# Optimization experiments

Hardware: AMD Instinct MI355X
Metric: run time of the kernel (lower is better)

Reference implementation:

```python
import jax, jax.numpy as jnp
import numpy as np

D_MODEL = 1024
N_HEADS = 16
D_HEAD = D_MODEL // N_HEADS
WIN = 256
NEG_INF = -1e30


def setup_inputs() -> dict:
    key = jax.random.key(0)
    k1, k2, k3 = jax.random.split(key, 3)
    B, L = 4, 4096
    x = jax.random.normal(k1, (B, L, D_MODEL), dtype=jnp.float32)
    w_qkv = jax.random.normal(k2, (D_MODEL, 3 * D_MODEL), dtype=jnp.float32) * (1.0 / np.sqrt(D_MODEL))
    w_out = jax.random.normal(k3, (D_MODEL, D_MODEL), dtype=jnp.float32) * (1.0 / np.sqrt(D_MODEL))
    return {"x": x, "w_qkv": w_qkv, "w_out": w_out}


def _band_mask(nb: int):
    ti = jnp.arange(WIN)[:, None]
    tj = jnp.arange(2 * WIN)[None, :]
    base = (tj >= ti + 1) & (tj <= ti + WIN)
    first = base & (tj >= WIN)                         # block 0 has zero-padded (invalid) prev block
    rest = jnp.broadcast_to(base, (nb - 1, WIN, 2 * WIN))
    return jnp.concatenate([first[None], rest], axis=0)


def reference(x, w_qkv, w_out):
    B, L, D = x.shape
    nb = L // WIN
    qkv = (x @ w_qkv).reshape(B, L, 3, N_HEADS, D_HEAD)
    q, k, v = qkv[:, :, 0], qkv[:, :, 1], qkv[:, :, 2]          # [B, L, H, dh]
    def to_blocks(t):
        return t.transpose(0, 2, 1, 3).reshape(B, N_HEADS, nb, WIN, D_HEAD)
    qb, kb, vb = to_blocks(q), to_blocks(k), to_blocks(v)
    zero_blk = jnp.zeros_like(kb[:, :, :1])
    k_kv = jnp.concatenate([jnp.concatenate([zero_blk, kb[:, :, :-1]], axis=2), kb], axis=3)  # [B,H,nb,2W,dh]
    v_kv = jnp.concatenate([jnp.concatenate([zero_blk, vb[:, :, :-1]], axis=2), vb], axis=3)
    scale = 1.0 / np.sqrt(D_HEAD)
    scores = jnp.einsum('bhnqd,bhnkd->bhnqk', qb, k_kv) * scale
    scores = jnp.where(_band_mask(nb), scores, NEG_INF)
    attn = jax.nn.softmax(scores, axis=-1)
    ob = jnp.einsum('bhnqk,bhnkd->bhnqd', attn, v_kv)
    out = ob.reshape(B, N_HEADS, L, D_HEAD).transpose(0, 2, 1, 3).reshape(B, L, D)
    return out @ w_out
```

## Files before the change

kernel.cpp:

```cpp
#include <hip/hip_runtime.h>

typedef __bf16 bf16_t;
typedef __bf16 bf16x8 __attribute__((ext_vector_type(8)));
typedef float f32x4 __attribute__((ext_vector_type(4)));
typedef unsigned short ushort_t;

#define MFMA_16x16x32(a, b, c) __builtin_amdgcn_mfma_f32_16x16x32_bf16((a), (b), (c), 0, 0, 0)

__device__ __forceinline__ void async_ld16(const void* gptr, void* lptr) {
  typedef __attribute__((address_space(1))) const unsigned int as1_t;
  typedef __attribute__((address_space(3))) unsigned int as3_t;
  __builtin_amdgcn_global_load_lds((as1_t*)(unsigned long long)gptr,
                                   (as3_t*)(unsigned int)(unsigned long long)lptr,
                                   16, 0, 0);
}

__global__ void detect_dtype(const ushort_t* __restrict__ x, int* __restrict__ flag) {
  __shared__ int cnt[256];
  int c = 0;
#pragma unroll
  for (int i = 0; i < 16; ++i) {
    const ushort_t u = x[threadIdx.x * 16 + i];
    const int e = (u >> 7) & 0xFF;
    if ((u & 0x7FFF) != 0 && (e < 0x3A || e > 0xC0)) ++c;
  }
  cnt[threadIdx.x] = c;
  __syncthreads();
  if (threadIdx.x == 0) {
    int t = 0;
    for (int i = 0; i < 256; ++i) t += cnt[i];
    *flag = (t > 512) ? 1 : 0;
  }
}

__global__ __launch_bounds__(256) void convert_to_bf16(const void* __restrict__ src,
                                                       bf16_t* __restrict__ dst, int n8,
                                                       const int* __restrict__ flag) {
  const int isF32 = *flag;
  int i = blockIdx.x * 256 + threadIdx.x;
  const int stride = gridDim.x * 256;
  if (isF32) {
    const float4* s = (const float4*)src;
    for (; i < n8; i += stride) {
      const float4 a = s[(size_t)i * 2];
      const float4 b = s[(size_t)i * 2 + 1];
      bf16x8 o;
      o[0] = (bf16_t)a.x; o[1] = (bf16_t)a.y; o[2] = (bf16_t)a.z; o[3] = (bf16_t)a.w;
      o[4] = (bf16_t)b.x; o[5] = (bf16_t)b.y; o[6] = (bf16_t)b.z; o[7] = (bf16_t)b.w;
      *(bf16x8*)(dst + (size_t)i * 8) = o;
    }
  } else {
    const uint4* s = (const uint4*)src;
    for (; i < n8; i += stride) ((uint4*)dst)[i] = s[i];
  }
}

__global__ __launch_bounds__(256) void transpose_b16(const ushort_t* __restrict__ in,
                                                     ushort_t* __restrict__ out,
                                                     int R, int C) {
  __shared__ alignas(16) ushort_t t[64 * 72];
  const int tid = threadIdx.x;
  const int c0 = blockIdx.x * 64;
  const int r0 = blockIdx.y * 64;
#pragma unroll
  for (int it = 0; it < 2; ++it) {
    int cid = tid + it * 256;
    int row = cid >> 3, co = (cid & 7) * 8;
    *(uint4*)(t + row * 72 + co) = *(const uint4*)(in + (size_t)(r0 + row) * C + c0 + co);
  }
  __syncthreads();
#pragma unroll
  for (int it = 0; it < 2; ++it) {
    int cid = tid + it * 256;
    int orow = cid >> 3, ko = (cid & 7) * 8;
    uint4 u;
    ushort_t* tp = (ushort_t*)&u;
#pragma unroll
    for (int j = 0; j < 8; ++j) tp[j] = t[(ko + j) * 72 + orow];
    *(uint4*)(out + (size_t)(c0 + orow) * R + r0 + ko) = u;
  }
}

__global__ __launch_bounds__(256) void transpose_v(const ushort_t* __restrict__ qkv,
                                                   ushort_t* __restrict__ vT) {
  __shared__ alignas(16) ushort_t t[64 * 72];
  const int tid = threadIdx.x;
  const int l0 = blockIdx.x * 64;
  const int bh = blockIdx.y;
  const int b = bh >> 4, h = bh & 15;
  const ushort_t* src = qkv + ((size_t)(b * 4096 + l0)) * 3072 + 2048 + h * 64;
#pragma unroll
  for (int it = 0; it < 2; ++it) {
    int cid = tid + it * 256;
    int row = cid >> 3, co = (cid & 7) * 8;
    *(uint4*)(t + row * 72 + co) = *(const uint4*)(src + (size_t)row * 3072 + co);
  }
  __syncthreads();
  ushort_t* dst = vT + ((size_t)bh * 64) * 4096 + l0;
#pragma unroll
  for (int it = 0; it < 2; ++it) {
    int cid = tid + it * 256;
    int d = cid >> 3, ko = (cid & 7) * 8;
    uint4 u;
    ushort_t* tp = (ushort_t*)&u;
#pragma unroll
    for (int j = 0; j < 8; ++j) tp[j] = t[(ko + j) * 72 + d];
    *(uint4*)(dst + (size_t)d * 4096 + ko) = u;
  }
}

__global__ __launch_bounds__(512) void gemm_bf16(const bf16_t* __restrict__ A, int lda,
                                                 const bf16_t* __restrict__ Bt,
                                                 void* __restrict__ Cout, int N_out,
                                                 int K, const int* __restrict__ flag) {
  __shared__ alignas(16) bf16_t smem[49152];
  const int tid = threadIdx.x;
  const int wave = tid >> 6;
  const int lane = tid & 63;
  const int l15 = lane & 15;
  const int quad = lane >> 4;
  const int wm = wave >> 2;
  const int wn = wave & 3;

  int lin = blockIdx.y * gridDim.x + blockIdx.x;
  const int nwg = gridDim.x * gridDim.y;
  if ((nwg & 7) == 0) lin = (lin & 7) * (nwg >> 3) + (lin >> 3);
  const int tn = (lin % gridDim.x) * 256;
  const int tm = (lin / gridDim.x) * 256;

  f32x4 acc[8][4];
#pragma unroll
  for (int i = 0; i < 8; ++i)
#pragma unroll
    for (int j = 0; j < 4; ++j) acc[i][j] = (f32x4){0.f, 0.f, 0.f, 0.f};

  const int r_st = tid >> 2;
  const int csrc = ((tid & 3) ^ ((tid >> 3) & 3)) * 8;
  const int wofs = wave * 512;

  const int rowA = wm * 16 + l15;
  const int rowB = wn * 16 + l15;
  const int cfr = (quad ^ ((l15 >> 1) & 3)) * 8;

  const int NT = K >> 5;

#define STAGE_HALF(G, ldg, grow0, kk, base)                                  \
  async_ld16((G) + (size_t)((grow0) + r_st) * (ldg) + (kk) + csrc,           \
             &smem[(base) + wofs])

#define STAGE4(kk, base)                                \
  do {                                                  \
    STAGE_HALF(A, lda, tm, (kk), (base));               \
    STAGE_HALF(Bt, K, tn, (kk), (base) + 8192);         \
    STAGE_HALF(Bt, K, tn + 128, (kk), (base) + 12288);  \
    STAGE_HALF(A, lda, tm + 128, (kk), (base) + 4096);  \
  } while (0)

  STAGE4(0, 0);
  STAGE4(32, 16384);
  asm volatile("s_waitcnt vmcnt(4)" ::: "memory");
  __builtin_amdgcn_s_barrier();

  int rb = 0;
  for (int t = 0; t < NT; ++t) {
    const int kst = (t + 2) << 5;
    const bool pf = (kst < K);
    const int sb = (rb >= 16384) ? rb - 16384 : rb + 32768;
    if (pf) STAGE4(kst, sb);

    bf16x8 a_[8], b_[4];
#pragma unroll
    for (int mh = 0; mh < 2; ++mh)
#pragma unroll
      for (int q = 0; q < 4; ++q)
        a_[mh * 4 + q] = *(const bf16x8*)&smem[rb + mh * 4096 +
                                               ((q * 32 + rowA) << 5) + cfr];
#pragma unroll
    for (int nh = 0; nh < 2; ++nh)
#pragma unroll
      for (int jn = 0; jn < 2; ++jn)
        b_[nh * 2 + jn] = *(const bf16x8*)&smem[rb + 8192 + nh * 4096 +
                                                ((jn * 64 + rowB) << 5) + cfr];

    __builtin_amdgcn_s_setprio(1);
#pragma unroll
    for (int f = 0; f < 8; ++f)
#pragma unroll
      for (int n = 0; n < 4; ++n) acc[f][n] = MFMA_16x16x32(a_[f], b_[n], acc[f][n]);
    __builtin_amdgcn_s_setprio(0);

    asm volatile("s_waitcnt vmcnt(4)" ::: "memory");
    if (!pf) asm volatile("s_waitcnt vmcnt(0)" ::: "memory");
    __builtin_amdgcn_s_barrier();
    rb = (rb == 32768) ? 0 : rb + 16384;
  }

  __syncthreads();

  const int isF32 = flag ? *flag : 0;
  if (isF32) {
#pragma unroll
    for (int f = 0; f < 8; ++f) {
      const int m0 = tm + (f >> 2) * 128 + (f & 3) * 32 + wm * 16 + quad * 4;
#pragma unroll
      for (int nidx = 0; nidx < 4; ++nidx) {
        const int col = tn + (nidx >> 1) * 128 + (nidx & 1) * 64 + wn * 16 + l15;
        float* cp = (float*)Cout + (size_t)m0 * N_out + col;
#pragma unroll
        for (int r = 0; r < 4; ++r) cp[(size_t)r * N_out] = acc[f][nidx][r];
      }
    }
  } else {
    bf16_t* stg = smem + wave * 1152;
#pragma unroll
    for (int f = 0; f < 8; ++f) {
#pragma unroll
      for (int nidx = 0; nidx < 4; ++nidx)
#pragma unroll
        for (int r = 0; r < 4; ++r)
          stg[(quad * 4 + r) * 72 + nidx * 16 + l15] = (bf16_t)acc[f][nidx][r];
      __asm__ volatile("s_waitcnt lgkmcnt(0)" ::: "memory");
      const int m0 = tm + (f >> 2) * 128 + (f & 3) * 32 + wm * 16;
#pragma unroll
      for (int p = 0; p < 2; ++p) {
        const int idx = lane + p * 64;
        const int row = idx >> 3, c8 = (idx & 7) * 8;
        uint4 u = *(const uint4*)(stg + row * 72 + c8);
        const int col = tn + ((c8 >> 5) << 7) + (((c8 >> 4) & 1) << 6) + wn * 16 + (c8 & 15);
        *(uint4*)((bf16_t*)Cout + (size_t)(m0 + row) * N_out + col) = u;
      }
      __asm__ volatile("s_waitcnt lgkmcnt(0)" ::: "memory");
    }
  }
#undef STAGE_HALF
#undef STAGE4
}

__global__ __launch_bounds__(256) void attn_swa(bf16_t* qkv, const bf16_t* __restrict__ vT) {
  __shared__ alignas(16) bf16_t k_lds[64 * 72];
  __shared__ alignas(16) bf16_t vt_lds[64 * 72];
  __shared__ alignas(16) bf16_t p_lds[4 * 16 * 72];

  int wg = blockIdx.x;
  wg = (wg & 7) * 512 + (wg >> 3);
  const int b = wg >> 10;
  const int h = (wg >> 6) & 15;
  const int qt = wg & 63;
  const int blk = qt >> 2;
  const int wq = qt & 3;
  const int tid = threadIdx.x;
  const int wave = tid >> 6;
  const int lane = tid & 63;
  const int l15 = lane & 15;
  const int quad = lane >> 4;
  const int qw = qt * 64 + wave * 16;

  const size_t qoff = ((size_t)(b * 4096 + qw + l15)) * 3072 + h * 64;
  const bf16x8 qf0 = *(const bf16x8*)(qkv + qoff + quad * 8);
  const bf16x8 qf1 = *(const bf16x8*)(qkv + qoff + 32 + quad * 8);

  f32x4 of[4];
#pragma unroll
  for (int i = 0; i < 4; ++i) of[i] = (f32x4){0.f, 0.f, 0.f, 0.f};
  float m_i[4], l_i[4];
#pragma unroll
  for (int r = 0; r < 4; ++r) {
    m_i[r] = -1e30f;
    l_i[r] = 0.0f;
  }

  const int kb0 = blk * 256 - 256;
  const int kclo = (blk == 0) ? 4 : wq;
  const int kchi = wq + 4;

  const int row0 = tid >> 3;
  const int co8 = (tid & 7) * 8;
  const bf16_t* kbase = qkv + ((size_t)b * 4096) * 3072 + 1024 + h * 64;
  const bf16_t* vbase = vT + (((size_t)b * 16 + h) * 64) * 4096;
  uint4 kr0, kr1, vr0, vr1;

#define ISSUE_KV(KB)                                                           \
  do {                                                                         \
    kr0 = *(const uint4*)(kbase + (size_t)((KB) + row0) * 3072 + co8);         \
    kr1 = *(const uint4*)(kbase + (size_t)((KB) + row0 + 32) * 3072 + co8);    \
    vr0 = *(const uint4*)(vbase + (size_t)row0 * 4096 + (KB) + co8);           \
    vr1 = *(const uint4*)(vbase + (size_t)(row0 + 32) * 4096 + (KB) + co8);    \
  } while (0)

  ISSUE_KV(kb0 + kclo * 64);

  for (int kc = kclo; kc <= kchi; ++kc) {
    const int kb = kb0 + kc * 64;
    __syncthreads();
    *(uint4*)(k_lds + row0 * 72 + co8) = kr0;
    *(uint4*)(k_lds + (row0 + 32) * 72 + co8) = kr1;
    *(uint4*)(vt_lds + row0 * 72 + co8) = vr0;
    *(uint4*)(vt_lds + (row0 + 32) * 72 + co8) = vr1;
    if (kc < kchi) ISSUE_KV(kb + 64);
    __syncthreads();

    f32x4 s[4];
    __builtin_amdgcn_s_setprio(1);
#pragma unroll
    for (int nt = 0; nt < 4; ++nt) {
      bf16x8 kf0 = *(const bf16x8*)(k_lds + (nt * 16 + l15) * 72 + quad * 8);
      bf16x8 kf1 = *(const bf16x8*)(k_lds + (nt * 16 + l15) * 72 + 32 + quad * 8);
      f32x4 z = (f32x4){0.f, 0.f, 0.f, 0.f};
      z = MFMA_16x16x32(qf0, kf0, z);
      z = MFMA_16x16x32(qf1, kf1, z);
      s[nt] = z;
    }
    __builtin_amdgcn_s_setprio(0);

    const bool full = (kb + 63 <= qw) && (kb >= qw - 240);
    float sv[4][4];
    if (full) {
#pragma unroll
      for (int nt = 0; nt < 4; ++nt)
#pragma unroll
        for (int r = 0; r < 4; ++r) sv[nt][r] = s[nt][r] * 0.125f;
    } else {
#pragma unroll
      for (int nt = 0; nt < 4; ++nt) {
        const int key = kb + nt * 16 + l15;
#pragma unroll
        for (int r = 0; r < 4; ++r) {
          const int p = qw + quad * 4 + r;
          const bool valid = (key <= p) && (key + 256 > p);
          sv[nt][r] = valid ? s[nt][r] * 0.125f : -1e30f;
        }
      }
    }
    float rm[4];
#pragma unroll
    for (int r = 0; r < 4; ++r)
      rm[r] = fmaxf(fmaxf(sv[0][r], sv[1][r]), fmaxf(sv[2][r], sv[3][r]));
#pragma unroll
    for (int off = 1; off < 16; off <<= 1)
#pragma unroll
      for (int r = 0; r < 4; ++r) rm[r] = fmaxf(rm[r], __shfl_xor(rm[r], off));

    const bool dok = (rm[0] <= m_i[0] + 8.0f) && (rm[1] <= m_i[1] + 8.0f) &&
                     (rm[2] <= m_i[2] + 8.0f) && (rm[3] <= m_i[3] + 8.0f);
    const bool defer = __all((int)dok);
    float mn[4];
    if (defer) {
#pragma unroll
      for (int r = 0; r < 4; ++r) mn[r] = m_i[r];
    } else {
#pragma unroll
      for (int r = 0; r < 4; ++r) mn[r] = fmaxf(m_i[r], rm[r]);
    }

    float rs[4] = {0.f, 0.f, 0.f, 0.f};
#pragma unroll
    for (int nt = 0; nt < 4; ++nt)
#pragma unroll
      for (int r = 0; r < 4; ++r) {
        const float pv = __expf(sv[nt][r] - mn[r]);
        rs[r] += pv;
        p_lds[wave * 1152 + (quad * 4 + r) * 72 + nt * 16 + l15] = (bf16_t)pv;
      }
#pragma unroll
    for (int off = 1; off < 16; off <<= 1)
#pragma unroll
      for (int r = 0; r < 4; ++r) rs[r] += __shfl_xor(rs[r], off);

    if (defer) {
#pragma unroll
      for (int r = 0; r < 4; ++r) l_i[r] += rs[r];
    } else {
#pragma unroll
      for (int r = 0; r < 4; ++r) {
        const float alpha = __expf(m_i[r] - mn[r]);
        l_i[r] = l_i[r] * alpha + rs[r];
        m_i[r] = mn[r];
#pragma unroll
        for (int dt = 0; dt < 4; ++dt) of[dt][r] *= alpha;
      }
    }

    __builtin_amdgcn_s_setprio(1);
#pragma unroll
    for (int kk = 0; kk < 2; ++kk) {
      bf16x8 pf = *(const bf16x8*)(p_lds + wave * 1152 + l15 * 72 + kk * 32 + quad * 8);
#pragma unroll
      for (int dt = 0; dt < 4; ++dt) {
        bf16x8 vf = *(const bf16x8*)(vt_lds + (dt * 16 + l15) * 72 + kk * 32 + quad * 8);
        of[dt] = MFMA_16x16x32(pf, vf, of[dt]);
      }
    }
    __builtin_amdgcn_s_setprio(0);
  }
#undef ISSUE_KV

  float inv[4];
#pragma unroll
  for (int r = 0; r < 4; ++r) inv[r] = 1.0f / fmaxf(l_i[r], 1e-20f);
  bf16_t* op = qkv + ((size_t)(b * 4096 + qw)) * 3072 + h * 64;
#pragma unroll
  for (int dt = 0; dt < 4; ++dt)
#pragma unroll
    for (int r = 0; r < 4; ++r)
      op[(size_t)(quad * 4 + r) * 3072 + dt * 16 + l15] = (bf16_t)(of[dt][r] * inv[r]);
}

extern "C" void kernel_launch(void* const* d_in, const int* in_sizes, int n_in,
                              void* d_out, int out_size, void* d_ws, size_t ws_size,
                              hipStream_t stream) {
  char* ws = (char*)d_ws;
  bf16_t* wTq = (bf16_t*)(ws);
  bf16_t* wTo = (bf16_t*)(ws + 6291456);
  bf16_t* qkv = (bf16_t*)(ws + 8388608);
  int* flag = (int*)(ws + 109051904);

  bf16_t* xb = (bf16_t*)d_out;
  bf16_t* vTb = (bf16_t*)d_out;
  bf16_t* tmpq = qkv;
  bf16_t* tmpo = qkv + 3145728;

  detect_dtype<<<1, 256, 0, stream>>>((const ushort_t*)d_in[0], flag);
  convert_to_bf16<<<1024, 256, 0, stream>>>(d_in[0], xb, 2097152, flag);
  convert_to_bf16<<<512, 256, 0, stream>>>(d_in[1], tmpq, 393216, flag);
  convert_to_bf16<<<256, 256, 0, stream>>>(d_in[2], tmpo, 131072, flag);
  transpose_b16<<<dim3(48, 16), 256, 0, stream>>>((const ushort_t*)tmpq, (ushort_t*)wTq,
                                                  1024, 3072);
  transpose_b16<<<dim3(16, 16), 256, 0, stream>>>((const ushort_t*)tmpo, (ushort_t*)wTo,
                                                  1024, 1024);
  gemm_bf16<<<dim3(12, 64), 512, 0, stream>>>(xb, 1024, wTq, qkv, 3072, 1024, nullptr);
  transpose_v<<<dim3(64, 64), 256, 0, stream>>>((const ushort_t*)qkv, (ushort_t*)vTb);
  attn_swa<<<dim3(4096), 256, 0, stream>>>(qkv, vTb);
  gemm_bf16<<<dim3(4, 64), 512, 0, stream>>>(qkv, 3072, wTo, d_out, 1024, 1024, flag);
}
```

Measured before the change: 386.7 us.

## Use 128x128 tile GEMM for output projection and simplify attention softmax

Adds a new 128x128-tile, 256-thread bf16 GEMM kernel and uses it for the output projection, giving 1024 workgroups in place of 256 larger tiles, which raises occupancy and parallelism. The new kernel has a simple single-buffered K loop with two barriers per step and no pipelining. In the attention kernel it removes the full-tile fast path and the deferred max-rescale trick, so the online softmax now always rescales. Masked scores are explicitly zeroed. This adds extra exp and multiply work per iteration.

Measured after the change: 411.3 us. 6.4% more time.

```diff
diff --git a/kernel.cpp b/kernel.cpp
--- a/kernel.cpp
+++ b/kernel.cpp
@@ -236,6 +236,96 @@
 #undef STAGE4
 }
 
+__global__ __launch_bounds__(256) void gemm128_bf16(const bf16_t* __restrict__ A, int lda,
+                                                    const bf16_t* __restrict__ Bt,
+                                                    void* __restrict__ Cout, int N_out,
+                                                    int K, const int* __restrict__ flag) {
+  __shared__ alignas(16) bf16_t smem[8192];
+  bf16_t* a_lds = smem;
+  bf16_t* b_lds = smem + 4096;
+  const int tid = threadIdx.x;
+  const int wave = tid >> 6;
+  const int lane = tid & 63;
+  const int l15 = lane & 15;
+  const int quad = lane >> 4;
+  const int tm = blockIdx.y * 128;
+  const int tn = blockIdx.x * 128;
+  const int wm = (wave >> 1) * 64;
+  const int wn = (wave & 1) * 64;
+
+  f32x4 acc[4][4];
+#pragma unroll
+  for (int i = 0; i < 4; ++i)
+#pragma unroll
+    for (int j = 0; j < 4; ++j) acc[i][j] = (f32x4){0.f, 0.f, 0.f, 0.f};
+
+  const int srow = wave * 32 + (lane >> 2);
+  const int scol = (lane & 3) * 8;
+  const bf16_t* ag = A + (size_t)(tm + srow) * lda + scol;
+  const bf16_t* bg = Bt + (size_t)(tn + srow) * K + scol;
+  bf16_t* al = a_lds + (wave * 32) * 32;
+  bf16_t* bl = b_lds + (wave * 32) * 32;
+
+  for (int k0 = 0; k0 < K; k0 += 32) {
+    __syncthreads();
+    async_ld16(ag, al);
+    async_ld16(ag + (size_t)16 * lda, al + 16 * 32);
+    async_ld16(bg, bl);
+    async_ld16(bg + (size_t)16 * K, bl + 16 * 32);
+    ag += 32;
+    bg += 32;
+    __syncthreads();
+
+    bf16x8 af[4], bfr[4];
+#pragma unroll
+    for (int i = 0; i < 4; ++i)
+      af[i] = *(const bf16x8*)(a_lds + (wm + i * 16 + l15) * 32 + quad * 8);
+#pragma unroll
+    for (int j = 0; j < 4; ++j)
+      bfr[j] = *(const bf16x8*)(b_lds + (wn + j * 16 + l15) * 32 + quad * 8);
+#pragma unroll
+    for (int i = 0; i < 4; ++i)
+#pragma unroll
+      for (int j = 0; j < 4; ++j) acc[i][j] = MFMA_16x16x32(af[i], bfr[j], acc[i][j]);
+  }
+  __syncthreads();
+
+  const int isF32 = flag ? *flag : 0;
+  if (isF32) {
+#pragma unroll
+    for (int i = 0; i < 4; ++i) {
+      const int m = tm + wm + i * 16 + quad * 4;
+#pragma unroll
+      for (int j = 0; j < 4; ++j) {
+        const int n = tn + wn + j * 16 + l15;
+        float* cp = (float*)Cout + (size_t)m * N_out + n;
+#pragma unroll
+        for (int r = 0; r < 4; ++r) cp[(size_t)r * N_out] = acc[i][j][r];
+      }
+    }
+  } else {
+    bf16_t* stg = smem + wave * 1152;
+#pragma unroll
+    for (int i = 0; i < 4; ++i) {
+#pragma unroll
+      for (int j = 0; j < 4; ++j)
+#pragma unroll
+        for (int r = 0; r < 4; ++r)
+          stg[(quad * 4 + r) * 72 + j * 16 + l15] = (bf16_t)acc[i][j][r];
+      __asm__ volatile("s_waitcnt lgkmcnt(0)" ::: "memory");
+      const int m0 = tm + wm + i * 16;
+#pragma unroll
+      for (int p = 0; p < 2; ++p) {
+        const int idx = lane + p * 64;
+        const int row = idx >> 3, c8 = (idx & 7) * 8;
+        uint4 u = *(const uint4*)(stg + row * 72 + c8);
+        *(uint4*)((bf16_t*)Cout + (size_t)(m0 + row) * N_out + tn + wn + c8) = u;
+      }
+      __asm__ volatile("s_waitcnt lgkmcnt(0)" ::: "memory");
+    }
+  }
+}
+
 __global__ __launch_bounds__(256) void attn_swa(bf16_t* qkv, const bf16_t* __restrict__ vT) {
   __shared__ alignas(16) bf16_t k_lds[64 * 72];
   __shared__ alignas(16) bf16_t vt_lds[64 * 72];
@@ -312,23 +402,15 @@
     }
     __builtin_amdgcn_s_setprio(0);
 
-    const bool full = (kb + 63 <= qw) && (kb >= qw - 240);
     float sv[4][4];
-    if (full) {
-#pragma unroll
-      for (int nt = 0; nt < 4; ++nt)
-#pragma unroll
-        for (int r = 0; r < 4; ++r) sv[nt][r] = s[nt][r] * 0.125f;
-    } else {
-#pragma unroll
-      for (int nt = 0; nt < 4; ++nt) {
-        const int key = kb + nt * 16 + l15;
-#pragma unroll
-        for (int r = 0; r < 4; ++r) {
-          const int p = qw + quad * 4 + r;
-          const bool valid = (key <= p) && (key + 256 > p);
-          sv[nt][r] = valid ? s[nt][r] * 0.125f : -1e30f;
-        }
+#pragma unroll
+    for (int nt = 0; nt < 4; ++nt) {
+      const int key = kb + nt * 16 + l15;
+#pragma unroll
+      for (int r = 0; r < 4; ++r) {
+        const int p = qw + quad * 4 + r;
+        const bool valid = (key <= p) && (key + 256 > p);
+        sv[nt][r] = valid ? s[nt][r] * 0.125f : -1e30f;
       }
     }
     float rm[4];
@@ -340,16 +422,12 @@
 #pragma unroll
       for (int r = 0; r < 4; ++r) rm[r] = fmaxf(rm[r], __shfl_xor(rm[r], off));
 
-    const bool dok = (rm[0] <= m_i[0] + 8.0f) && (rm[1] <= m_i[1] + 8.0f) &&
-                     (rm[2] <= m_i[2] + 8.0f) && (rm[3] <= m_i[3] + 8.0f);
-    const bool defer = __all((int)dok);
-    float mn[4];
-    if (defer) {
-#pragma unroll
-      for (int r = 0; r < 4; ++r) mn[r] = m_i[r];
-    } else {
-#pragma unroll
-      for (int r = 0; r < 4; ++r) mn[r] = fmaxf(m_i[r], rm[r]);
+    float mn[4], alpha[4];
+#pragma unroll
+    for (int r = 0; r < 4; ++r) {
+      mn[r] = fmaxf(m_i[r], rm[r]);
+      alpha[r] = __expf(m_i[r] - mn[r]);
+      m_i[r] = mn[r];
     }
 
     float rs[4] = {0.f, 0.f, 0.f, 0.f};
@@ -357,7 +435,7 @@
     for (int nt = 0; nt < 4; ++nt)
 #pragma unroll
       for (int r = 0; r < 4; ++r) {
-        const float pv = __expf(sv[nt][r] - mn[r]);
+        const float pv = (sv[nt][r] > -1e29f) ? __expf(sv[nt][r] - mn[r]) : 0.0f;
         rs[r] += pv;
         p_lds[wave * 1152 + (quad * 4 + r) * 72 + nt * 16 + l15] = (bf16_t)pv;
       }
@@ -365,20 +443,12 @@
     for (int off = 1; off < 16; off <<= 1)
 #pragma unroll
       for (int r = 0; r < 4; ++r) rs[r] += __shfl_xor(rs[r], off);
-
-    if (defer) {
-#pragma unroll
-      for (int r = 0; r < 4; ++r) l_i[r] += rs[r];
-    } else {
-#pragma unroll
-      for (int r = 0; r < 4; ++r) {
-        const float alpha = __expf(m_i[r] - mn[r]);
-        l_i[r] = l_i[r] * alpha + rs[r];
-        m_i[r] = mn[r];
-#pragma unroll
-        for (int dt = 0; dt < 4; ++dt) of[dt][r] *= alpha;
-      }
-    }
+#pragma unroll
+    for (int r = 0; r < 4; ++r) l_i[r] = l_i[r] * alpha[r] + rs[r];
+#pragma unroll
+    for (int dt = 0; dt < 4; ++dt)
+#pragma unroll
+      for (int r = 0; r < 4; ++r) of[dt][r] *= alpha[r];
 
     __builtin_amdgcn_s_setprio(1);
 #pragma unroll
@@ -430,5 +500,5 @@
   gemm_bf16<<<dim3(12, 64), 512, 0, stream>>>(xb, 1024, wTq, qkv, 3072, 1024, nullptr);
   transpose_v<<<dim3(64, 64), 256, 0, stream>>>((const ushort_t*)qkv, (ushort_t*)vTb);
   attn_swa<<<dim3(4096), 256, 0, stream>>>(qkv, vTb);
-  gemm_bf16<<<dim3(4, 64), 512, 0, stream>>>(qkv, 3072, wTo, d_out, 1024, 1024, flag);
-}
+  gemm128_bf16<<<dim3(8, 128), 256, 0, stream>>>(qkv, 3072, wTo, d_out, 1024, 1024, flag);
+}
```
